# Performance work log

Measured on AMD Instinct MI355X. Metric: run time of the kernel, lower is better.

The kernel has to match this reference:

```python
import jax, jax.numpy as jnp
import numpy as np

K = 1  # number of items to sample exactly
B, N = 512, 8192


def log1mexp(x):
    # log(1 - exp(x)) for x <= 0, numerically stable (Maechler 2012)
    return jnp.where(x > -jnp.log(2.0), jnp.log(-jnp.expm1(x)), jnp.log1p(-jnp.exp(x)))


def logaddexp_c(x1, x2):
    # custom logaddexp matching the torch module (handles -inf == -inf ties)
    delta = jnp.where(x1 == x2, 0.0, x1 - x2)
    return jnp.maximum(x1, x2) + jax.nn.softplus(-jnp.abs(delta))


def dp_table(logp, logq, kk):
    # a[b, i, c] = log Pr(exactly c-1 successes among first i items); shape [B, n+1, kk+2]
    bsz = logp.shape[0]
    state0 = jnp.full((bsz, kk + 2), -jnp.inf, logp.dtype).at[:, 1].set(0.0)
    ninf_col = jnp.full((bsz, 1), -jnp.inf, logp.dtype)

    def step(state, xs):
        lp, lq = xs  # each [B]
        grown = logaddexp_c(state[:, :-1] + lp[:, None], state[:, 1:] + lq[:, None])
        new = jnp.concatenate([ninf_col, grown], axis=1)
        return new, new

    _, rows = jax.lax.scan(step, state0, (logp.T, logq.T))  # rows: [n, B, kk+2]
    return jnp.concatenate([state0[None], rows], axis=0).transpose(1, 0, 2)


def sample_scan(a, logp, noise):
    # reverse DP sampling pass; a: [B, n+1, C], logp/noise: [B, n]
    bsz, np1, C = a.shape
    n = np1 - 1
    kcol = C - 1  # == K + 1 in table-column coordinates
    ap = a[:, :-1, :][:, ::-1].transpose(1, 0, 2)  # [n, B, C], row i-1 for i=n..1
    ac = a[:, 1:, :][:, ::-1].transpose(1, 0, 2)   # [n, B, C], row i   for i=n..1
    lp_rev = logp[:, ::-1].T                        # [n, B]
    u_rev = noise[:, ::-1].T                        # [n, B]

    def step(j, xs):
        ap_r, ac_r, lp_t, u_t = xs
        p = jnp.take_along_axis(ap_r, (j - 1)[:, None], axis=1)[:, 0]
        z = jnp.take_along_axis(ac_r, j[:, None], axis=1)[:, 0]
        p = jnp.minimum(p + lp_t - z, 0.0)  # conditional log-prob, clamp fp round-off
        q = log1mexp(p)
        X = (u_t < jax.nn.sigmoid(p - q)).astype(logp.dtype)  # Bernoulli(logits=p-q)
        j = jnp.where(X > 0, j - 1, j)
        return j, X

    j0 = jnp.full((bsz,), kcol, jnp.int32)
    _, Xs = jax.lax.scan(step, j0, (ap, ac, lp_rev, u_rev))  # Xs: [n, B]
    return Xs[::-1].T  # [B, n]


def setup_inputs() -> dict:
    key = jax.random.key(0)
    k1, k2 = jax.random.split(key)
    logits = jax.random.normal(k1, (B, N), dtype=jnp.float32)
    noise = jax.random.uniform(k2, (B, N), dtype=jnp.float32)
    return {"logits": logits, "noise": noise}


def reference(logits, noise):
    logp = jnp.minimum(jax.nn.log_sigmoid(logits), -1e-7)  # clamped log_sigmoid
    logq = log1mexp(logp)
    a = dp_table(logp, logq, K)       # [B, N+1, K+2]
    return sample_scan(a, logp, noise)  # [B, N] in {0,1}
```

## Files before the change

### kernel.cpp

```cpp
#include <hip/hip_runtime.h>
#include <math.h>
#include <stdint.h>

#define NB 512
#define NI 8192
#define NG (NI / 4)
#define NLOG2 0.69314718055994530942f

__device__ __forceinline__ float log1mexp_f(float x) {
    return (x > -NLOG2) ? logf(-expm1f(x)) : log1pf(-expf(x));
}

__device__ float g_P[(size_t)NB * NI];

#define TB 64
#define TK 16
__global__ __launch_bounds__(256) void prep_kernel(const float* __restrict__ logits,
                                                   float* __restrict__ Alp,
                                                   float* __restrict__ Blq) {
    __shared__ float4 lp_t[TB][TK + 1];
    __shared__ float4 lq_t[TB][TK + 1];
    int bx = blockIdx.x;
    int tb = (bx & 7) * TB;
    int tkb = (bx >> 3) * TK;
    int t = threadIdx.x;

    int kl = t & 15;
    int rl0 = t >> 4;
#pragma unroll
    for (int r = 0; r < 4; ++r) {
        int row_local = r * 16 + rl0;
        float4 x4 = *(const float4*)&logits[(size_t)(tb + row_local) * NI + (size_t)(tkb + kl) * 4];
        float4 lp4, lq4;
        const float* xs = &x4.x;
        float* lps = &lp4.x;
        float* lqs = &lq4.x;
#pragma unroll
        for (int j = 0; j < 4; ++j) {
            float x = xs[j];
            float lp = -(fmaxf(-x, 0.0f) + log1pf(expf(-fabsf(x))));
            lp = fminf(lp, -1e-7f);
            lps[j] = lp;
            lqs[j] = log1mexp_f(lp);
        }
        lp_t[row_local][kl] = lp4;
        lq_t[row_local][kl] = lq4;
    }
    __syncthreads();

    int bl = t & 63;
    int kw0 = t >> 6;
#pragma unroll
    for (int w = 0; w < 4; ++w) {
        int k_local = w * 4 + kw0;
        size_t dst = (size_t)(tkb + k_local) * NB + (size_t)(tb + bl);
        ((float4*)Alp)[dst] = lp_t[bl][k_local];
        ((float4*)Blq)[dst] = lq_t[bl][k_local];
    }
}

__device__ __forceinline__ void scan_step_p(float lp, float lq, float& S0, float& S1,
                                            float& po) {
    const float L2E = 1.44269504088896340736f;
    const float LN2 = 0.69314718055994530942f;
    float x1 = S0 + lp;
    float x2 = S1 + lq;
    float d  = x1 - x2;
    float m  = fmaxf(x1, x2);
    float z  = fabsf(d) * -L2E;
    float e  = __builtin_amdgcn_exp2f(z);
    float a  = 1.0f + e;
    float l  = __builtin_amdgcn_logf(a);
    S1 = fmaf(l, LN2, m);
    S0 = S0 + lq;
    po = fminf(x1 - S1, 0.0f);
}

#define CHR 8
#define WV 4

__global__ __launch_bounds__(256, 1) void scan_kernel(const float* __restrict__ A,
                                                      const float* __restrict__ B) {
    int lane = threadIdx.x & 63;
    int w = threadIdx.x >> 6;
    int row = blockIdx.x * 64 + lane;
    const float4* Ap = (const float4*)A;
    const float4* Bp = (const float4*)B;
    float4* Pp = (float4*)g_P;

    __shared__ float S0s[64], S1s[64];
    if (threadIdx.x < 64) { S0s[threadIdx.x] = 0.0f; S1s[threadIdx.x] = -INFINITY; }

    float4 lpR[CHR], lqR[CHR];
#pragma unroll
    for (int j = 0; j < CHR; ++j) {
        lpR[j] = Ap[(size_t)(w * CHR + j) * NB + row];
        lqR[j] = Bp[(size_t)(w * CHR + j) * NB + row];
    }
    __syncthreads();

    const int NCHUNK = NG / CHR;
    for (int c = 0; c < NCHUNK; ++c) {
        if ((c & (WV - 1)) == w) {
            float S0 = S0s[lane];
            float S1 = S1s[lane];
#pragma unroll
            for (int j = 0; j < CHR; ++j) {
                float4 p4;
                scan_step_p(lpR[j].x, lqR[j].x, S0, S1, p4.x);
                scan_step_p(lpR[j].y, lqR[j].y, S0, S1, p4.y);
                scan_step_p(lpR[j].z, lqR[j].z, S0, S1, p4.z);
                scan_step_p(lpR[j].w, lqR[j].w, S0, S1, p4.w);
                Pp[(size_t)(c * CHR + j) * NB + row] = p4;
            }
            S0s[lane] = S0;
            S1s[lane] = S1;
            int cn = c + WV;
            if (cn < NCHUNK) {
#pragma unroll
                for (int j = 0; j < CHR; ++j) {
                    lpR[j] = Ap[(size_t)(cn * CHR + j) * NB + row];
                    lqR[j] = Bp[(size_t)(cn * CHR + j) * NB + row];
                }
            }
        }
        __syncthreads();
    }
}

__global__ __launch_bounds__(256) void decide_kernel(const float* __restrict__ noise,
                                                     float* __restrict__ out) {
    int row = blockIdx.x;
    const float4* pp = (const float4*)g_P;
    const float4* ur = (const float4*)(noise + (size_t)row * NI);
    float4* outr = (float4*)(out + (size_t)row * NI);
    int tid = threadIdx.x;

    int best = -1;
#pragma unroll
    for (int k = 0; k < NG / 256; ++k) {
        int g = tid + k * 256;
        float4 p4 = pp[(size_t)g * NB + row];
        float4 u = ur[g];
#pragma unroll
        for (int j = 0; j < 4; ++j) {
            float p = (&p4.x)[j];
            float q = log1mexp_f(p);
            float z = p - q;
            float prob = 1.0f / (1.0f + expf(-z));
            if ((&u.x)[j] < prob) {
                int i = 4 * g + j;
                best = (i > best) ? i : best;
            }
        }
    }

#pragma unroll
    for (int off = 32; off > 0; off >>= 1) {
        int o = __shfl_down(best, off);
        best = (o > best) ? o : best;
    }
    __shared__ int lds[4];
    __shared__ int sel_s;
    int wid = tid >> 6;
    if ((tid & 63) == 0) lds[wid] = best;
    __syncthreads();
    if (tid == 0) {
        int s01 = (lds[0] > lds[1]) ? lds[0] : lds[1];
        int s23 = (lds[2] > lds[3]) ? lds[2] : lds[3];
        sel_s = (s01 > s23) ? s01 : s23;
    }
    __syncthreads();
    int sel = sel_s;

#pragma unroll
    for (int k = 0; k < NG / 256; ++k) {
        int g = tid + k * 256;
        int i0 = 4 * g;
        float4 v;
        v.x = (i0 == sel) ? 1.0f : 0.0f;
        v.y = (i0 + 1 == sel) ? 1.0f : 0.0f;
        v.z = (i0 + 2 == sel) ? 1.0f : 0.0f;
        v.w = (i0 + 3 == sel) ? 1.0f : 0.0f;
        outr[g] = v;
    }
}

extern "C" void kernel_launch(void* const* d_in, const int* in_sizes, int n_in,
                              void* d_out, int out_size, void* d_ws, size_t ws_size,
                              hipStream_t stream) {
    (void)in_sizes; (void)n_in; (void)out_size; (void)ws_size;
    const float* logits = (const float*)d_in[0];
    const float* noise = (const float*)d_in[1];
    float* out = (float*)d_out;
    float* A = (float*)d_ws;

    prep_kernel<<<8 * (NG / TK), 256, 0, stream>>>(logits, A, out);
    scan_kernel<<<8, 256, 0, stream>>>(A, out);
    decide_kernel<<<NB, 256, 0, stream>>>(noise, out);
}
```

Before: 418.3 us.

## Rewrite DP scan as single-wave blocks with async LDS ring buffer

The forward scan kernel drops its four-wave round-robin design, which needed a __syncthreads per chunk and handed state through shared memory. It now runs one wave per block, and each lane carries two independent rows whose recurrence steps are interleaved to hide exp/log latency. Inputs are streamed with global_load_lds into a three-slot shared-memory ring, and manual vmcnt waits let the prefetch of chunk c+2 overlap the compute of chunk c. The launch drops from 8 blocks to 4, so fewer CUs are used. The hand-tuned wait counts depend on how stores and loads are counted together in vmcnt, which is a correctness risk.

```diff
diff --git a/kernel.cpp b/kernel.cpp
--- a/kernel.cpp
+++ b/kernel.cpp
@@ -76,55 +76,81 @@
     po = fminf(x1 - S1, 0.0f);
 }
 
-#define CHR 8
-#define WV 4
-
-__global__ __launch_bounds__(256, 1) void scan_kernel(const float* __restrict__ A,
-                                                      const float* __restrict__ B) {
-    int lane = threadIdx.x & 63;
-    int w = threadIdx.x >> 6;
-    int row = blockIdx.x * 64 + lane;
+#define CH 8
+#define SLOTS 3
+
+#define GLOAD_LDS(gp, lp) \
+    __builtin_amdgcn_global_load_lds( \
+        (const __attribute__((address_space(1))) void*)(gp), \
+        (__attribute__((address_space(3))) void*)(lp), 16, 0, 0)
+
+__global__ __launch_bounds__(64, 1) void scan_kernel(const float* __restrict__ A,
+                                                     const float* __restrict__ B) {
+    int lane = threadIdx.x;
+    int row0 = blockIdx.x * 64 + lane;
+    int row1 = row0 + 256;
     const float4* Ap = (const float4*)A;
     const float4* Bp = (const float4*)B;
     float4* Pp = (float4*)g_P;
 
-    __shared__ float S0s[64], S1s[64];
-    if (threadIdx.x < 64) { S0s[threadIdx.x] = 0.0f; S1s[threadIdx.x] = -INFINITY; }
-
-    float4 lpR[CHR], lqR[CHR];
-#pragma unroll
-    for (int j = 0; j < CHR; ++j) {
-        lpR[j] = Ap[(size_t)(w * CHR + j) * NB + row];
-        lqR[j] = Bp[(size_t)(w * CHR + j) * NB + row];
-    }
-    __syncthreads();
-
-    const int NCHUNK = NG / CHR;
+    __shared__ float4 sA0[SLOTS][CH][64];
+    __shared__ float4 sB0[SLOTS][CH][64];
+    __shared__ float4 sA1[SLOTS][CH][64];
+    __shared__ float4 sB1[SLOTS][CH][64];
+
+    float S0a = 0.0f, S1a = -INFINITY;
+    float S0b = 0.0f, S1b = -INFINITY;
+
+#pragma unroll
+    for (int j = 0; j < CH; ++j) {
+        GLOAD_LDS(&Ap[(size_t)(0 * CH + j) * NB + row0], &sA0[0][j][0]);
+        GLOAD_LDS(&Bp[(size_t)(0 * CH + j) * NB + row0], &sB0[0][j][0]);
+        GLOAD_LDS(&Ap[(size_t)(0 * CH + j) * NB + row1], &sA1[0][j][0]);
+        GLOAD_LDS(&Bp[(size_t)(0 * CH + j) * NB + row1], &sB1[0][j][0]);
+    }
+#pragma unroll
+    for (int j = 0; j < CH; ++j) {
+        GLOAD_LDS(&Ap[(size_t)(1 * CH + j) * NB + row0], &sA0[1][j][0]);
+        GLOAD_LDS(&Bp[(size_t)(1 * CH + j) * NB + row0], &sB0[1][j][0]);
+        GLOAD_LDS(&Ap[(size_t)(1 * CH + j) * NB + row1], &sA1[1][j][0]);
+        GLOAD_LDS(&Bp[(size_t)(1 * CH + j) * NB + row1], &sB1[1][j][0]);
+    }
+    asm volatile("s_waitcnt vmcnt(32)" ::: "memory");
+    __builtin_amdgcn_sched_barrier(0);
+
+    const int NCHUNK = NG / CH;
+    int s = 0;
     for (int c = 0; c < NCHUNK; ++c) {
-        if ((c & (WV - 1)) == w) {
-            float S0 = S0s[lane];
-            float S1 = S1s[lane];
-#pragma unroll
-            for (int j = 0; j < CHR; ++j) {
-                float4 p4;
-                scan_step_p(lpR[j].x, lqR[j].x, S0, S1, p4.x);
-                scan_step_p(lpR[j].y, lqR[j].y, S0, S1, p4.y);
-                scan_step_p(lpR[j].z, lqR[j].z, S0, S1, p4.z);
-                scan_step_p(lpR[j].w, lqR[j].w, S0, S1, p4.w);
-                Pp[(size_t)(c * CHR + j) * NB + row] = p4;
-            }
-            S0s[lane] = S0;
-            S1s[lane] = S1;
-            int cn = c + WV;
-            if (cn < NCHUNK) {
-#pragma unroll
-                for (int j = 0; j < CHR; ++j) {
-                    lpR[j] = Ap[(size_t)(cn * CHR + j) * NB + row];
-                    lqR[j] = Bp[(size_t)(cn * CHR + j) * NB + row];
-                }
-            }
-        }
-        __syncthreads();
+        int sn = (s >= 1) ? (s - 1) : (s + 2);
+        int cn = (c + 2) & (NCHUNK - 1);
+#pragma unroll
+        for (int j = 0; j < CH; ++j) {
+            GLOAD_LDS(&Ap[(size_t)(cn * CH + j) * NB + row0], &sA0[sn][j][0]);
+            GLOAD_LDS(&Bp[(size_t)(cn * CH + j) * NB + row0], &sB0[sn][j][0]);
+            GLOAD_LDS(&Ap[(size_t)(cn * CH + j) * NB + row1], &sA1[sn][j][0]);
+            GLOAD_LDS(&Bp[(size_t)(cn * CH + j) * NB + row1], &sB1[sn][j][0]);
+        }
+#pragma unroll
+        for (int j = 0; j < CH; ++j) {
+            float4 lp0 = sA0[s][j][lane];
+            float4 lq0 = sB0[s][j][lane];
+            float4 lp1 = sA1[s][j][lane];
+            float4 lq1 = sB1[s][j][lane];
+            float4 p0, p1;
+            scan_step_p(lp0.x, lq0.x, S0a, S1a, p0.x);
+            scan_step_p(lp1.x, lq1.x, S0b, S1b, p1.x);
+            scan_step_p(lp0.y, lq0.y, S0a, S1a, p0.y);
+            scan_step_p(lp1.y, lq1.y, S0b, S1b, p1.y);
+            scan_step_p(lp0.z, lq0.z, S0a, S1a, p0.z);
+            scan_step_p(lp1.z, lq1.z, S0b, S1b, p1.z);
+            scan_step_p(lp0.w, lq0.w, S0a, S1a, p0.w);
+            scan_step_p(lp1.w, lq1.w, S0b, S1b, p1.w);
+            Pp[(size_t)(c * CH + j) * NB + row0] = p0;
+            Pp[(size_t)(c * CH + j) * NB + row1] = p1;
+        }
+        asm volatile("s_waitcnt vmcnt(48)" ::: "memory");
+        __builtin_amdgcn_sched_barrier(0);
+        s = (s >= 2) ? 0 : (s + 1);
     }
 }
 
@@ -196,6 +222,6 @@
     float* A = (float*)d_ws;
 
     prep_kernel<<<8 * (NG / TK), 256, 0, stream>>>(logits, A, out);
-    scan_kernel<<<8, 256, 0, stream>>>(A, out);
+    scan_kernel<<<4, 64, 0, stream>>>(A, out);
     decide_kernel<<<NB, 256, 0, stream>>>(noise, out);
 }
```

Result: slower. 870.3 us (+108.1%).
